# Performance work log

Measured on AMD Instinct MI355X. Metric: run time of the kernel, lower is better.

The kernel has to match this reference:

```python
import jax, jax.numpy as jnp
import numpy as np

NI = 256
RED = 16

def setup_inputs() -> dict:
    key = jax.random.key(0)
    k1, k2, k3 = jax.random.split(key, 3)
    B, C, L = 32, NI, 8192
    x = jax.random.normal(k1, (B, C, L), dtype=jnp.float32)
    H = NI // RED  # 16
    # torch.nn.Linear weights: [out_features, in_features], kaiming-uniform-ish scale
    W1 = jax.random.uniform(k2, (H, C), dtype=jnp.float32, minval=-1.0, maxval=1.0) / np.sqrt(C)
    W2 = jax.random.uniform(k3, (C, H), dtype=jnp.float32, minval=-1.0, maxval=1.0) / np.sqrt(H)
    return {"x": x, "W1": W1, "W2": W2}

def reference(x, W1, W2):
    # squeeze: global average pool over sequence -> [B, C]
    y = jnp.mean(x, axis=2)
    # excite: tiny bottleneck MLP -> per-channel gates in (0,1)
    h = jax.nn.relu(jnp.einsum('bc,hc->bh', y, W1))
    g = jax.nn.sigmoid(jnp.einsum('bh,ch->bc', h, W2))
    # scale: channel-wise recalibration
    return x * g[:, :, None]
```

## Files before the change

### kernel.cpp

```cpp
#include <hip/hip_runtime.h>
#include <math.h>

#define B 32
#define C 256
#define L 8192
#define H 16

typedef float v4f __attribute__((ext_vector_type(4)));

__global__ __launch_bounds__(256) void k_mean(const float* __restrict__ x,
                                              float* __restrict__ y) {
    const int row = blockIdx.x;
    const v4f* xr = (const v4f*)(x + (size_t)row * L);
    float s = 0.f;
#pragma unroll
    for (int i = 0; i < 8; ++i) {
        v4f v = xr[threadIdx.x + i * 256];
        s += (v.x + v.y) + (v.z + v.w);
    }
#pragma unroll
    for (int off = 32; off > 0; off >>= 1)
        s += __shfl_down(s, off, 64);
    __shared__ float ws[4];
    const int lane = threadIdx.x & 63;
    const int wave = threadIdx.x >> 6;
    if (lane == 0) ws[wave] = s;
    __syncthreads();
    if (threadIdx.x == 0) {
        float t = (ws[0] + ws[1]) + (ws[2] + ws[3]);
        y[row] = t * (1.0f / (float)L);
    }
}

__global__ __launch_bounds__(256) void k_mlp(const float* __restrict__ y,
                                             const float* __restrict__ W1,
                                             const float* __restrict__ W2,
                                             float* __restrict__ g) {
    const int b = blockIdx.x;
    __shared__ float ys[C];
    __shared__ float part[16][H + 1];
    __shared__ float hs[H];
    ys[threadIdx.x] = y[b * C + threadIdx.x];
    __syncthreads();
    {
        const int j = threadIdx.x & 15;
        const int k = threadIdx.x >> 4;
        const float* w = W1 + j * C + k * 16;
        const float* yy = ys + k * 16;
        float s = 0.f;
#pragma unroll
        for (int c = 0; c < 16; ++c) s += yy[c] * w[c];
        part[k][j] = s;
    }
    __syncthreads();
    if (threadIdx.x < H) {
        float s = 0.f;
#pragma unroll
        for (int k = 0; k < 16; ++k) s += part[k][threadIdx.x];
        hs[threadIdx.x] = fmaxf(s, 0.f);
    }
    __syncthreads();
    float s = 0.f;
    const float* w2 = W2 + threadIdx.x * H;
#pragma unroll
    for (int j = 0; j < H; ++j) s += hs[j] * w2[j];
    g[b * C + threadIdx.x] = 1.0f / (1.0f + __expf(-s));
}

__global__ __launch_bounds__(256) void k_scale(const float* __restrict__ x,
                                               const float* __restrict__ g,
                                               float* __restrict__ out) {
    const int row = blockIdx.x;
    const float gg = g[row];
    const v4f* xr = (const v4f*)(x + (size_t)row * L);
    v4f* orow = (v4f*)(out + (size_t)row * L);
#pragma unroll
    for (int i = 0; i < 8; ++i) {
        v4f v = xr[threadIdx.x + i * 256];
        v.x *= gg; v.y *= gg; v.z *= gg; v.w *= gg;
        __builtin_nontemporal_store(v, &orow[threadIdx.x + i * 256]);
    }
}

extern "C" void kernel_launch(void* const* d_in, const int* in_sizes, int n_in,
                              void* d_out, int out_size, void* d_ws, size_t ws_size,
                              hipStream_t stream) {
    const float* x  = (const float*)d_in[0];
    const float* W1 = (const float*)d_in[1];
    const float* W2 = (const float*)d_in[2];
    float* out = (float*)d_out;

    float* y = (float*)d_ws;
    float* g = y + B * C;

    k_mean<<<B * C, 256, 0, stream>>>(x, y);
    k_mlp<<<B, 256, 0, stream>>>(y, W1, W2, g);
    k_scale<<<B * C, 256, 0, stream>>>(x, g, out);
}
```

Before: 474.9 us.

## Fuse excitation MLP into scale kernel with eight rows per block

Removes the separate MLP kernel launch and gate buffer. Each scale block now handles eight consecutive channel rows, recomputes the batch's bottleneck hidden layer itself, and computes the eight gates it needs before scaling those rows. This saves one launch and its serialization gap, but repeats the W1 matvec across the 32 blocks of each batch and puts a short serial compute prologue ahead of the streaming loop.

```diff
diff --git a/kernel.cpp b/kernel.cpp
--- a/kernel.cpp
+++ b/kernel.cpp
@@ -5,6 +5,9 @@
 #define C 256
 #define L 8192
 #define H 16
+
+#define RPB  8
+#define NBLK (B * C / RPB)
 
 typedef float v4f __attribute__((ext_vector_type(4)));
 
@@ -32,20 +35,28 @@
     }
 }
 
-__global__ __launch_bounds__(256) void k_mlp(const float* __restrict__ y,
-                                             const float* __restrict__ W1,
-                                             const float* __restrict__ W2,
-                                             float* __restrict__ g) {
-    const int b = blockIdx.x;
+__global__ __launch_bounds__(256) void k_mlp_scale(
+    const float* __restrict__ x,
+    const float* __restrict__ y,
+    const float* __restrict__ W1,
+    const float* __restrict__ W2,
+    float* __restrict__ out)
+{
+    const int tid  = threadIdx.x;
+    const int row0 = blockIdx.x * RPB;
+    const int b    = row0 / C;
+
     __shared__ float ys[C];
     __shared__ float part[16][H + 1];
     __shared__ float hs[H];
-    ys[threadIdx.x] = y[b * C + threadIdx.x];
+    __shared__ float gs[RPB];
+
+    ys[tid] = y[b * C + tid];
     __syncthreads();
     {
-        const int j = threadIdx.x & 15;
-        const int k = threadIdx.x >> 4;
-        const float* w = W1 + j * C + k * 16;
+        const int j = tid & 15;
+        const int k = tid >> 4;
+        const float* w  = W1 + j * C + k * 16;
         const float* yy = ys + k * 16;
         float s = 0.f;
 #pragma unroll
@@ -53,32 +64,34 @@
         part[k][j] = s;
     }
     __syncthreads();
-    if (threadIdx.x < H) {
+    if (tid < H) {
         float s = 0.f;
 #pragma unroll
-        for (int k = 0; k < 16; ++k) s += part[k][threadIdx.x];
-        hs[threadIdx.x] = fmaxf(s, 0.f);
+        for (int k = 0; k < 16; ++k) s += part[k][tid];
+        hs[tid] = fmaxf(s, 0.f);
     }
     __syncthreads();
-    float s = 0.f;
-    const float* w2 = W2 + threadIdx.x * H;
+    if (tid < RPB) {
+        const int c = (row0 + tid) & (C - 1);
+        const float* w2 = W2 + c * H;
+        float s = 0.f;
 #pragma unroll
-    for (int j = 0; j < H; ++j) s += hs[j] * w2[j];
-    g[b * C + threadIdx.x] = 1.0f / (1.0f + __expf(-s));
-}
+        for (int j = 0; j < H; ++j) s += hs[j] * w2[j];
+        gs[tid] = 1.0f / (1.0f + __expf(-s));
+    }
+    __syncthreads();
 
-__global__ __launch_bounds__(256) void k_scale(const float* __restrict__ x,
-                                               const float* __restrict__ g,
-                                               float* __restrict__ out) {
-    const int row = blockIdx.x;
-    const float gg = g[row];
-    const v4f* xr = (const v4f*)(x + (size_t)row * L);
-    v4f* orow = (v4f*)(out + (size_t)row * L);
+    for (int r = 0; r < RPB; ++r) {
+        const int row = row0 + r;
+        const float gg = gs[r];
+        const v4f* xr = (const v4f*)(x + (size_t)row * L);
+        v4f* orow = (v4f*)(out + (size_t)row * L);
 #pragma unroll
-    for (int i = 0; i < 8; ++i) {
-        v4f v = xr[threadIdx.x + i * 256];
-        v.x *= gg; v.y *= gg; v.z *= gg; v.w *= gg;
-        __builtin_nontemporal_store(v, &orow[threadIdx.x + i * 256]);
+        for (int i = 0; i < 8; ++i) {
+            v4f v = xr[tid + i * 256];
+            v.x *= gg; v.y *= gg; v.z *= gg; v.w *= gg;
+            __builtin_nontemporal_store(v, &orow[tid + i * 256]);
+        }
     }
 }
 
@@ -91,9 +104,7 @@
     float* out = (float*)d_out;
 
     float* y = (float*)d_ws;
-    float* g = y + B * C;
 
     k_mean<<<B * C, 256, 0, stream>>>(x, y);
-    k_mlp<<<B, 256, 0, stream>>>(y, W1, W2, g);
-    k_scale<<<B * C, 256, 0, stream>>>(x, g, out);
+    k_mlp_scale<<<NBLK, 256, 0, stream>>>(x, y, W1, W2, out);
 }
```

Result: no change. 475.3 us (+0.1%).
